# Optimization experiments

Hardware: AMD Instinct MI355X
Metric: run time of the kernel (lower is better)

The kernel has to match this reference:

```python
import jax, jax.numpy as jnp
import numpy as np

NEG_SLOPE = 0.01  # F.leaky_relu default
EPS = 1e-12       # F.normalize default eps

def _lrelu(h):
    return jnp.where(h > 0, h, NEG_SLOPE * h)

def setup_inputs() -> dict:
    key = jax.random.key(0)
    ks = jax.random.split(key, 16)
    N, E, D = 100000, 800000, 64
    x = jax.random.normal(ks[0], (N, D), dtype=jnp.float32)
    src = jax.random.randint(ks[1], (E,), 0, N, dtype=jnp.int32)
    dst = jax.random.randint(ks[2], (E,), 0, N, dtype=jnp.int32)
    def lin(k, fo, fi):
        k1, k2 = jax.random.split(k)
        s = 1.0 / np.sqrt(fi)
        w = jax.random.uniform(k1, (fo, fi), jnp.float32, -s, s)
        b = jax.random.uniform(k2, (fo,), jnp.float32, -s, s)
        return w, b
    w1, b1 = lin(ks[3], 256, D)
    w2, b2 = lin(ks[4], 128, 256)
    w3, b3 = lin(ks[5], 64, 128)
    w4, b4 = lin(ks[6], 1, 64)
    w_self, _ = lin(ks[7], D, D)   # SAGEConv fc_self (no bias)
    w_neigh, _ = lin(ks[8], D, D)  # SAGEConv fc_neigh (no bias)
    bias = jnp.zeros((D,), jnp.float32)  # SAGEConv bias param
    return dict(x=x, src=src, dst=dst, w1=w1, b1=b1, w2=w2, b2=b2,
                w3=w3, b3=b3, w4=w4, b4=b4,
                w_self=w_self, w_neigh=w_neigh, bias=bias)

def reference(x, src, dst, w1, b1, w2, b2, w3, b3, w4, b4, w_self, w_neigh, bias):
    N = x.shape[0]
    # per-edge score MLP on (h_u - h_v)
    d = x[src] - x[dst]                       # [E, D]
    h = _lrelu(d @ w1.T + b1)                 # [E, 256]
    h = _lrelu(h @ w2.T + b2)                 # [E, 128]
    h = _lrelu(h @ w3.T + b3)                 # [E, 64]
    e = jax.nn.sigmoid(h @ w4.T + b4)         # [E, 1]
    # SAGEConv 'mean' with edge weights: mean over incoming edges of e * x_src
    msg = e * x[src]                          # [E, D]
    s = jax.ops.segment_sum(msg, dst, num_segments=N)               # [N, D]
    deg = jax.ops.segment_sum(jnp.ones((src.shape[0],), x.dtype), dst,
                              num_segments=N)                        # [N]
    neigh = s / jnp.maximum(deg, 1.0)[:, None]
    A = x @ w_self.T + neigh @ w_neigh.T + bias
    A = _lrelu(A)
    norm = jnp.maximum(jnp.linalg.norm(A, axis=1, keepdims=True), EPS)
    A = A / norm
    return A, e
```

## Files before the change

kernel.cpp:

```cpp
#include <hip/hip_runtime.h>
#include <hip/hip_bf16.h>

typedef unsigned short u16;
typedef unsigned int   u32;
typedef __attribute__((ext_vector_type(8))) short short8;
typedef __attribute__((ext_vector_type(4))) float f32x4;

__device__ __forceinline__ u16 f2bf(float f) {
  u32 u = __float_as_uint(f);
  u += 0x7FFFu + ((u >> 16) & 1u);
  return (u16)(u >> 16);
}
__device__ __forceinline__ float bf2f(u16 h) { return __uint_as_float(((u32)h) << 16); }
__device__ __forceinline__ u32 pk2(float lo, float hi) {
  union { __hip_bfloat162 h; u32 u; } c;
  c.h = __float22bfloat162_rn(make_float2(lo, hi));
  return c.u;
}
__device__ __forceinline__ float lrelu(float v) { return v > 0.f ? v : 0.01f * v; }

__host__ __device__ __forceinline__ int sig(int c) {
  return ((c >> 5) << 5) | ((c & 12) << 1) | (((c >> 4) & 1) << 2) | (c & 3);
}

union U8 { u32 w[4]; short8 v; };

#define MFMA16(A, B, C) __builtin_amdgcn_mfma_f32_16x16x32_bf16(A, B, C, 0, 0, 0)

#define W2_BASE 2048
#define W3_BASE 6144
#define NCHUNK8 7168


__global__ __launch_bounds__(1024) void edge_mlp(
    const float* __restrict__ x, const int* __restrict__ src, const int* __restrict__ dst,
    const short8* __restrict__ wcat,
    const float* __restrict__ b1p, const float* __restrict__ b2p, const float* __restrict__ b3p,
    const float* __restrict__ w4p, const float* __restrict__ b4,
    const int* __restrict__ rowptr, int* __restrict__ cursor,
    u16* __restrict__ msgbuf, float* __restrict__ eout, int E)
{
  __shared__ short8 ldsw[NCHUNK8];
  const int tid  = threadIdx.x;
  const int lane = tid & 63;
  const int wv   = tid >> 6;
  const int g    = lane >> 4;
  const int r    = lane & 15;
  const int eb   = (blockIdx.x * 16 + wv) * 32;
  const int e0   = eb + r, e1 = eb + 16 + r;
  const int ec0  = e0 < E ? e0 : E - 1;
  const int ec1  = e1 < E ? e1 : E - 1;
  const int sn0 = src[ec0], dn0 = dst[ec0];
  const int sn1 = src[ec1], dn1 = dst[ec1];
  const float b4v = b4[0];

  const float* xsr0 = x + (size_t)sn0 * 64 + 8 * g;
  const float* xdr0 = x + (size_t)dn0 * 64 + 8 * g;
  const float* xsr1 = x + (size_t)sn1 * 64 + 8 * g;
  const float* xdr1 = x + (size_t)dn1 * 64 + 8 * g;
  const float4 a0s0 = *(const float4*)(xsr0),      a0s1 = *(const float4*)(xsr0 + 4);
  const float4 a0s2 = *(const float4*)(xsr0 + 32), a0s3 = *(const float4*)(xsr0 + 36);
  const float4 a0d0 = *(const float4*)(xdr0),      a0d1 = *(const float4*)(xdr0 + 4);
  const float4 a0d2 = *(const float4*)(xdr0 + 32), a0d3 = *(const float4*)(xdr0 + 36);
  const float4 a1s0 = *(const float4*)(xsr1),      a1s1 = *(const float4*)(xsr1 + 4);
  const float4 a1s2 = *(const float4*)(xsr1 + 32), a1s3 = *(const float4*)(xsr1 + 36);
  const float4 a1d0 = *(const float4*)(xdr1),      a1d1 = *(const float4*)(xdr1 + 4);
  const float4 a1d2 = *(const float4*)(xdr1 + 32), a1d3 = *(const float4*)(xdr1 + 36);

  {
    const short8* gp = wcat + wv * 64 + lane;
    short8*       lp = ldsw + wv * 64;
#pragma unroll
    for (int i = 0; i < 7; i++) {
      __builtin_amdgcn_global_load_lds(
          (const __attribute__((address_space(1))) u32*)(gp + i * 1024),
          (__attribute__((address_space(3))) u32*)(lp + i * 1024), 16, 0, 0);
    }
  }
  __syncthreads();

  U8 bA0, bB0, bA1, bB1;
  bA0.w[0] = pk2(a0s0.x - a0d0.x, a0s0.y - a0d0.y);
  bA0.w[1] = pk2(a0s0.z - a0d0.z, a0s0.w - a0d0.w);
  bA0.w[2] = pk2(a0s1.x - a0d1.x, a0s1.y - a0d1.y);
  bA0.w[3] = pk2(a0s1.z - a0d1.z, a0s1.w - a0d1.w);
  bB0.w[0] = pk2(a0s2.x - a0d2.x, a0s2.y - a0d2.y);
  bB0.w[1] = pk2(a0s2.z - a0d2.z, a0s2.w - a0d2.w);
  bB0.w[2] = pk2(a0s3.x - a0d3.x, a0s3.y - a0d3.y);
  bB0.w[3] = pk2(a0s3.z - a0d3.z, a0s3.w - a0d3.w);
  bA1.w[0] = pk2(a1s0.x - a1d0.x, a1s0.y - a1d0.y);
  bA1.w[1] = pk2(a1s0.z - a1d0.z, a1s0.w - a1d0.w);
  bA1.w[2] = pk2(a1s1.x - a1d1.x, a1s1.y - a1d1.y);
  bA1.w[3] = pk2(a1s1.z - a1d1.z, a1s1.w - a1d1.w);
  bB1.w[0] = pk2(a1s2.x - a1d2.x, a1s2.y - a1d2.y);
  bB1.w[1] = pk2(a1s2.z - a1d2.z, a1s2.w - a1d2.w);
  bB1.w[2] = pk2(a1s3.x - a1d3.x, a1s3.y - a1d3.y);
  bB1.w[3] = pk2(a1s3.z - a1d3.z, a1s3.w - a1d3.w);

  u32 h1a[32], h1b[32];
  {
    const float* b1l = b1p + 4 * g;
#pragma unroll
    for (int t = 0; t < 16; t++) {
      short8 a0 = ldsw[(t * 2 + 0) * 64 + lane];
      short8 a1 = ldsw[(t * 2 + 1) * 64 + lane];
      f32x4 p = {}, q = {};
      p = MFMA16(a0, bA0.v, p); p = MFMA16(a1, bB0.v, p);
      q = MFMA16(a0, bA1.v, q); q = MFMA16(a1, bB1.v, q);
      float4 bb = *(const float4*)(b1l + 16 * t);
      h1a[2 * t]     = pk2(lrelu(p[0] + bb.x), lrelu(p[1] + bb.y));
      h1a[2 * t + 1] = pk2(lrelu(p[2] + bb.z), lrelu(p[3] + bb.w));
      h1b[2 * t]     = pk2(lrelu(q[0] + bb.x), lrelu(q[1] + bb.y));
      h1b[2 * t + 1] = pk2(lrelu(q[2] + bb.z), lrelu(q[3] + bb.w));
    }
  }

  u32 h2a[16], h2b[16];
  {
    const float* b2l = b2p + 4 * g;
#pragma unroll
    for (int t = 0; t < 8; t++) {
      f32x4 p = {}, q = {};
#pragma unroll
      for (int s = 0; s < 8; s++) {
        short8 a = ldsw[W2_BASE + (t * 8 + s) * 64 + lane];
        U8 f0, f1;
        f0.w[0] = h1a[4 * s + 0]; f0.w[1] = h1a[4 * s + 1];
        f0.w[2] = h1a[4 * s + 2]; f0.w[3] = h1a[4 * s + 3];
        f1.w[0] = h1b[4 * s + 0]; f1.w[1] = h1b[4 * s + 1];
        f1.w[2] = h1b[4 * s + 2]; f1.w[3] = h1b[4 * s + 3];
        p = MFMA16(a, f0.v, p);
        q = MFMA16(a, f1.v, q);
      }
      float4 bb = *(const float4*)(b2l + 16 * t);
      h2a[2 * t]     = pk2(lrelu(p[0] + bb.x), lrelu(p[1] + bb.y));
      h2a[2 * t + 1] = pk2(lrelu(p[2] + bb.z), lrelu(p[3] + bb.w));
      h2b[2 * t]     = pk2(lrelu(q[0] + bb.x), lrelu(q[1] + bb.y));
      h2b[2 * t + 1] = pk2(lrelu(q[2] + bb.z), lrelu(q[3] + bb.w));
    }
  }

  float dot0 = 0.f, dot1 = 0.f;
  {
    const float* b3l = b3p + 4 * g;
    const float* w4l = w4p + 4 * g;
#pragma unroll
    for (int t = 0; t < 4; t++) {
      f32x4 p = {}, q = {};
#pragma unroll
      for (int s = 0; s < 4; s++) {
        short8 a = ldsw[W3_BASE + (t * 4 + s) * 64 + lane];
        U8 f0, f1;
        f0.w[0] = h2a[4 * s + 0]; f0.w[1] = h2a[4 * s + 1];
        f0.w[2] = h2a[4 * s + 2]; f0.w[3] = h2a[4 * s + 3];
        f1.w[0] = h2b[4 * s + 0]; f1.w[1] = h2b[4 * s + 1];
        f1.w[2] = h2b[4 * s + 2]; f1.w[3] = h2b[4 * s + 3];
        p = MFMA16(a, f0.v, p);
        q = MFMA16(a, f1.v, q);
      }
      float4 bb = *(const float4*)(b3l + 16 * t);
      float4 ww = *(const float4*)(w4l + 16 * t);
      dot0 += lrelu(p[0] + bb.x) * ww.x + lrelu(p[1] + bb.y) * ww.y
            + lrelu(p[2] + bb.z) * ww.z + lrelu(p[3] + bb.w) * ww.w;
      dot1 += lrelu(q[0] + bb.x) * ww.x + lrelu(q[1] + bb.y) * ww.y
            + lrelu(q[2] + bb.z) * ww.z + lrelu(q[3] + bb.w) * ww.w;
    }
  }
  dot0 += __shfl_xor(dot0, 16); dot0 += __shfl_xor(dot0, 32);
  dot1 += __shfl_xor(dot1, 16); dot1 += __shfl_xor(dot1, 32);
  const float ev0 = 1.f / (1.f + __expf(-(dot0 + b4v)));
  const float ev1 = 1.f / (1.f + __expf(-(dot1 + b4v)));

  int pos0 = 0, pos1 = 0;
  if (g == 0) {
    if (e0 < E) { eout[e0] = ev0; pos0 = rowptr[dn0] + atomicAdd(&cursor[dn0], 1); }
    if (e1 < E) { eout[e1] = ev1; pos1 = rowptr[dn1] + atomicAdd(&cursor[dn1], 1); }
  }
  pos0 = __shfl(pos0, r);
  pos1 = __shfl(pos1, r);
  if (e0 < E) {
    u16* mp = msgbuf + (size_t)pos0 * 64 + g * 16;
    U8 m;
    m.w[0] = pk2(ev0 * a0s0.x, ev0 * a0s0.y);
    m.w[1] = pk2(ev0 * a0s0.z, ev0 * a0s0.w);
    m.w[2] = pk2(ev0 * a0s1.x, ev0 * a0s1.y);
    m.w[3] = pk2(ev0 * a0s1.z, ev0 * a0s1.w);
    *(short8*)(mp) = m.v;
    m.w[0] = pk2(ev0 * a0s2.x, ev0 * a0s2.y);
    m.w[1] = pk2(ev0 * a0s2.z, ev0 * a0s2.w);
    m.w[2] = pk2(ev0 * a0s3.x, ev0 * a0s3.y);
    m.w[3] = pk2(ev0 * a0s3.z, ev0 * a0s3.w);
    *(short8*)(mp + 8) = m.v;
  }
  if (e1 < E) {
    u16* mp = msgbuf + (size_t)pos1 * 64 + g * 16;
    U8 m;
    m.w[0] = pk2(ev1 * a1s0.x, ev1 * a1s0.y);
    m.w[1] = pk2(ev1 * a1s0.z, ev1 * a1s0.w);
    m.w[2] = pk2(ev1 * a1s1.x, ev1 * a1s1.y);
    m.w[3] = pk2(ev1 * a1s1.z, ev1 * a1s1.w);
    *(short8*)(mp) = m.v;
    m.w[0] = pk2(ev1 * a1s2.x, ev1 * a1s2.y);
    m.w[1] = pk2(ev1 * a1s2.z, ev1 * a1s2.w);
    m.w[2] = pk2(ev1 * a1s3.x, ev1 * a1s3.y);
    m.w[3] = pk2(ev1 * a1s3.z, ev1 * a1s3.w);
    *(short8*)(mp + 8) = m.v;
  }
}

__global__ void deg_hist(const int* __restrict__ dst, int* __restrict__ degi, int E)
{
  const int i = blockIdx.x * 256 + threadIdx.x;
  if (i < E) atomicAdd(&degi[dst[i]], 1);
}

__global__ void scan_part(const int* __restrict__ degi, int* __restrict__ rowptr,
                          int* __restrict__ bsum, int N)
{
  __shared__ int wsum[4];
  const int tid = threadIdx.x, lane = tid & 63, w = tid >> 6;
  const int base = blockIdx.x * 1024 + tid * 4;
  int d0 = 0, d1 = 0, d2 = 0, d3 = 0;
  if (base + 3 < N) {
    int4 v = *(const int4*)(degi + base);
    d0 = v.x; d1 = v.y; d2 = v.z; d3 = v.w;
  } else {
    if (base < N)     d0 = degi[base];
    if (base + 1 < N) d1 = degi[base + 1];
    if (base + 2 < N) d2 = degi[base + 2];
    if (base + 3 < N) d3 = degi[base + 3];
  }
  const int ts = d0 + d1 + d2 + d3;
  int sc = ts;
#pragma unroll
  for (int o = 1; o < 64; o <<= 1) { int v = __shfl_up(sc, o); if (lane >= o) sc += v; }
  if (lane == 63) wsum[w] = sc;
  __syncthreads();
  int woff = 0;
  for (int i = 0; i < w; i++) woff += wsum[i];
  const int ex = woff + sc - ts;
  if (base < N)     rowptr[base]     = ex;
  if (base + 1 < N) rowptr[base + 1] = ex + d0;
  if (base + 2 < N) rowptr[base + 2] = ex + d0 + d1;
  if (base + 3 < N) rowptr[base + 3] = ex + d0 + d1 + d2;
  if (tid == 255) bsum[blockIdx.x] = woff + sc;
}

__global__ void scan_bsum(int* __restrict__ bsum, int nb)
{
  __shared__ int wsum[4];
  const int tid = threadIdx.x, lane = tid & 63, w = tid >> 6;
  const int v = tid < nb ? bsum[tid] : 0;
  int sc = v;
#pragma unroll
  for (int o = 1; o < 64; o <<= 1) { int t = __shfl_up(sc, o); if (lane >= o) sc += t; }
  if (lane == 63) wsum[w] = sc;
  __syncthreads();
  int woff = 0;
  for (int i = 0; i < w; i++) woff += wsum[i];
  if (tid < nb) bsum[tid] = woff + sc - v;
}

__global__ void scan_add(int* __restrict__ rowptr, const int* __restrict__ bsum,
                         int* __restrict__ cursor, int N, int E)
{
  const int base = blockIdx.x * 1024 + threadIdx.x * 4;
  const int off = bsum[blockIdx.x];
#pragma unroll
  for (int i = 0; i < 4; i++)
    if (base + i < N) { rowptr[base + i] += off; cursor[base + i] = 0; }
  if (blockIdx.x == 0 && threadIdx.x == 0) rowptr[N] = E;
}

__global__ __launch_bounds__(256, 4) void node_agg_mfma(
    const float* __restrict__ x, const u16* __restrict__ msgbuf,
    const int* __restrict__ rowptr, const short8* __restrict__ wfin,
    const float* __restrict__ bias, float* __restrict__ A, int N)
{
  __shared__ short8 ldsW[1024];
  __shared__ float  nbuf[4][16][68];
  const int tid = threadIdx.x, wv = tid >> 6, lane = tid & 63;
  const int g = lane >> 4, r = lane & 15;
  for (int i = tid; i < 1024; i += 256) ldsW[i] = wfin[i];

  const int n0 = (blockIdx.x * 4 + wv) * 16;
  const int nr = (n0 + r) < N ? (n0 + r) : N - 1;
  const float* xp = x + (size_t)nr * 64 + 8 * g;
  const float4 xf0 = *(const float4*)(xp);
  const float4 xf1 = *(const float4*)(xp + 4);
  const float4 xf2 = *(const float4*)(xp + 32);
  const float4 xf3 = *(const float4*)(xp + 36);
  int rp = 0;
  if (lane < 17) rp = rowptr[min(n0 + lane, N)];
  const int cch = (((lane >> 3) & 1) << 5) | ((lane >> 4) << 3) | (lane & 7);
  for (int rr = 0; rr < 16; rr++) {
    const int s = __shfl(rp, rr);
    const int t = __shfl(rp, rr + 1);
    float acc = 0.f;
    for (int j = s; j < t; j += 4) {
      const int j1 = (j + 1 < t) ? j + 1 : j;
      const int j2 = (j + 2 < t) ? j + 2 : j;
      const int j3 = (j + 3 < t) ? j + 3 : j;
      const float v0 = bf2f(msgbuf[(size_t)j  * 64 + lane]);
      const float v1 = bf2f(msgbuf[(size_t)j1 * 64 + lane]);
      const float v2 = bf2f(msgbuf[(size_t)j2 * 64 + lane]);
      const float v3 = bf2f(msgbuf[(size_t)j3 * 64 + lane]);
      const float m1 = (j + 1 < t) ? 1.f : 0.f;
      const float m2 = (j + 2 < t) ? 1.f : 0.f;
      const float m3 = (j + 3 < t) ? 1.f : 0.f;
      acc += v0 + m1 * v1 + m2 * v2 + m3 * v3;
    }
    const float inv = 1.f / fmaxf((float)(t - s), 1.f);
    nbuf[wv][rr][cch] = acc * inv;
  }
  __syncthreads();

  U8 bf0, bf1, bf2q, bf3q;
  bf0.w[0] = pk2(xf0.x, xf0.y); bf0.w[1] = pk2(xf0.z, xf0.w);
  bf0.w[2] = pk2(xf1.x, xf1.y); bf0.w[3] = pk2(xf1.z, xf1.w);
  bf1.w[0] = pk2(xf2.x, xf2.y); bf1.w[1] = pk2(xf2.z, xf2.w);
  bf1.w[2] = pk2(xf3.x, xf3.y); bf1.w[3] = pk2(xf3.z, xf3.w);
  {
    const float* nb = nbuf[wv][r];
    const float4 n0v = *(const float4*)(nb + 8 * g);
    const float4 n1v = *(const float4*)(nb + 8 * g + 4);
    const float4 n2v = *(const float4*)(nb + 32 + 8 * g);
    const float4 n3v = *(const float4*)(nb + 32 + 8 * g + 4);
    bf2q.w[0] = pk2(n0v.x, n0v.y); bf2q.w[1] = pk2(n0v.z, n0v.w);
    bf2q.w[2] = pk2(n1v.x, n1v.y); bf2q.w[3] = pk2(n1v.z, n1v.w);
    bf3q.w[0] = pk2(n2v.x, n2v.y); bf3q.w[1] = pk2(n2v.z, n2v.w);
    bf3q.w[2] = pk2(n3v.x, n3v.y); bf3q.w[3] = pk2(n3v.z, n3v.w);
  }

  f32x4 acct[4] = {};
#pragma unroll
  for (int t = 0; t < 4; t++) {
    acct[t] = MFMA16(ldsW[(t * 4 + 0) * 64 + lane], bf0.v,  acct[t]);
    acct[t] = MFMA16(ldsW[(t * 4 + 1) * 64 + lane], bf1.v,  acct[t]);
    acct[t] = MFMA16(ldsW[(t * 4 + 2) * 64 + lane], bf2q.v, acct[t]);
    acct[t] = MFMA16(ldsW[(t * 4 + 3) * 64 + lane], bf3q.v, acct[t]);
  }

  f32x4 av[4];
  float ss = 0.f;
#pragma unroll
  for (int t = 0; t < 4; t++) {
    const float4 bb = *(const float4*)(bias + 16 * t + 4 * g);
    av[t][0] = lrelu(acct[t][0] + bb.x);
    av[t][1] = lrelu(acct[t][1] + bb.y);
    av[t][2] = lrelu(acct[t][2] + bb.z);
    av[t][3] = lrelu(acct[t][3] + bb.w);
    ss += av[t][0] * av[t][0] + av[t][1] * av[t][1]
        + av[t][2] * av[t][2] + av[t][3] * av[t][3];
  }
  ss += __shfl_xor(ss, 16); ss += __shfl_xor(ss, 32);
  const float rn = 1.f / fmaxf(sqrtf(ss), 1e-12f);
  if (n0 + r < N) {
    float* ap = A + (size_t)(n0 + r) * 64 + 4 * g;
#pragma unroll
    for (int t = 0; t < 4; t++) {
      float4 o;
      o.x = av[t][0] * rn; o.y = av[t][1] * rn;
      o.z = av[t][2] * rn; o.w = av[t][3] * rn;
      *(float4*)(ap + 16 * t) = o;
    }
  }
}

__global__ void convert_w(const float* __restrict__ w1, const float* __restrict__ w2,
                          const float* __restrict__ w3,
                          const float* __restrict__ b1, const float* __restrict__ b2,
                          const float* __restrict__ b3, const float* __restrict__ w4,
                          const float* __restrict__ w_self, const float* __restrict__ w_neigh,
                          u16* __restrict__ wcat, u16* __restrict__ wfin,
                          float* __restrict__ b1p, float* __restrict__ b2p,
                          float* __restrict__ b3p, float* __restrict__ w4p)
{
  const int idx = blockIdx.x * 256 + threadIdx.x;
  if (idx < 57344) {
    const float* w; int K, nsteps, loc;
    if (idx < 16384)      { loc = idx;         w = w1; K = 64;  nsteps = 2; }
    else if (idx < 49152) { loc = idx - 16384; w = w2; K = 256; nsteps = 8; }
    else                  { loc = idx - 49152; w = w3; K = 128; nsteps = 4; }
    const int chunk = loc >> 9;
    const int lane  = (loc >> 3) & 63;
    const int j     = loc & 7;
    const int t = chunk / nsteps, s = chunk % nsteps;
    const int m = sig(t * 16 + (lane & 15));
    const int k = s * 32 + (lane >> 4) * 8 + j;
    wcat[idx] = f2bf(w[m * K + k]);
  } else if (idx < 65536) {
    const int o = idx - 57344;
    const int c = o >> 9, lane = (o >> 3) & 63, j = o & 7;
    const int t = c >> 2, s = c & 3;
    const int m = 16 * t + (lane & 15);
    const int k = 32 * s + ((lane >> 4) << 3) + j;
    wfin[o] = f2bf(k < 64 ? w_self[m * 64 + k] : w_neigh[m * 64 + (k - 64)]);
  }
  if (idx < 256) b1p[idx] = b1[sig(idx)];
  if (idx < 128) b2p[idx] = b2[sig(idx)];
  if (idx < 64)  { b3p[idx] = b3[sig(idx)]; w4p[idx] = w4[sig(idx)]; }
}

extern "C" void kernel_launch(void* const* d_in, const int* in_sizes, int n_in,
                              void* d_out, int out_size, void* d_ws, size_t ws_size,
                              hipStream_t stream)
{
  const float* x       = (const float*)d_in[0];
  const int*   src     = (const int*)d_in[1];
  const int*   dst     = (const int*)d_in[2];
  const float* w1      = (const float*)d_in[3];
  const float* b1      = (const float*)d_in[4];
  const float* w2      = (const float*)d_in[5];
  const float* b2      = (const float*)d_in[6];
  const float* w3      = (const float*)d_in[7];
  const float* b3      = (const float*)d_in[8];
  const float* w4      = (const float*)d_in[9];
  const float* b4      = (const float*)d_in[10];
  const float* w_self  = (const float*)d_in[11];
  const float* w_neigh = (const float*)d_in[12];
  const float* bias    = (const float*)d_in[13];

  const int N = in_sizes[0] / 64;
  const int E = in_sizes[1];

  float* A    = (float*)d_out;
  float* eout = (float*)d_out + (size_t)N * 64;

  char* ws = (char*)d_ws;
  size_t off = 0;
  auto alloc = [&](size_t bytes) {
    void* p = ws + off;
    off = (off + bytes + 255) & ~(size_t)255;
    return p;
  };
  int*    degi   = (int*)alloc((size_t)N * 4);
  int*    rowptr = (int*)alloc((size_t)(N + 1) * 4);
  int*    cursor = (int*)alloc((size_t)N * 4);
  int*    bsum   = (int*)alloc(1024 * 4);
  short8* wcat   = (short8*)alloc((size_t)57344 * 2);
  short8* wfin   = (short8*)alloc((size_t)8192 * 2);
  float*  b1p    = (float*)alloc(256 * 4);
  float*  b2p    = (float*)alloc(128 * 4);
  float*  b3p    = (float*)alloc(64 * 4);
  float*  w4p    = (float*)alloc(64 * 4);
  u16*    msgbuf = (u16*)alloc((size_t)E * 128);

  hipMemsetAsync(degi, 0, (size_t)N * sizeof(int), stream);

  convert_w<<<256, 256, 0, stream>>>(w1, w2, w3, b1, b2, b3, w4, w_self, w_neigh,
                                     (u16*)wcat, (u16*)wfin, b1p, b2p, b3p, w4p);

  deg_hist<<<(E + 255) / 256, 256, 0, stream>>>(dst, degi, E);

  const int nsb = (N + 1023) / 1024;
  scan_part<<<nsb, 256, 0, stream>>>(degi, rowptr, bsum, N);
  scan_bsum<<<1, 256, 0, stream>>>(bsum, nsb);
  scan_add<<<nsb, 256, 0, stream>>>(rowptr, bsum, cursor, N, E);

  const int nblk = (E + 511) / 512;
  edge_mlp<<<nblk, 1024, 0, stream>>>(x, src, dst, wcat, b1p, b2p, b3p, w4p, b4,
                                      rowptr, cursor, msgbuf, eout, E);

  const int nblk2 = (N + 63) / 64;
  node_agg_mfma<<<nblk2, 256, 0, stream>>>(x, msgbuf, rowptr, wfin, bias, A, N);
}
```

Measured before the change: 337.9 us.

## Stream layer-1 weights from global, shrink LDS and block size for occupancy

Layer-1 weights are now read directly from global memory (L2/L1 cached) with a one-step register prefetch, instead of being staged in LDS. The LDS staging of the layer-2 and layer-3 weights overlaps with layer-1 compute, and the barrier moves after layer 1. Blocks shrink from 1024 to 512 threads with launch_bounds(512,2), which cuts LDS per block so more blocks can be resident. Source features are packed to bf16 early so fewer fp32 registers stay live across the MLP. The trade-off is more global weight traffic per wave, slightly different message rounding (double bf16 rounding), and possible register spilling under the tighter bound.

```diff
diff --git a/kernel.cpp b/kernel.cpp
--- a/kernel.cpp
+++ b/kernel.cpp
@@ -17,6 +17,8 @@
   c.h = __float22bfloat162_rn(make_float2(lo, hi));
   return c.u;
 }
+__device__ __forceinline__ float lo16f(u32 u) { return __uint_as_float(u << 16); }
+__device__ __forceinline__ float hi16f(u32 u) { return __uint_as_float(u & 0xffff0000u); }
 __device__ __forceinline__ float lrelu(float v) { return v > 0.f ? v : 0.01f * v; }
 
 __host__ __device__ __forceinline__ int sig(int c) {
@@ -27,12 +29,11 @@
 
 #define MFMA16(A, B, C) __builtin_amdgcn_mfma_f32_16x16x32_bf16(A, B, C, 0, 0, 0)
 
-#define W2_BASE 2048
-#define W3_BASE 6144
-#define NCHUNK8 7168
-
-
-__global__ __launch_bounds__(1024) void edge_mlp(
+#define LDS_CHUNK8 5120
+#define LDS_W3     4096
+
+
+__global__ __launch_bounds__(512, 2) void edge_mlp(
     const float* __restrict__ x, const int* __restrict__ src, const int* __restrict__ dst,
     const short8* __restrict__ wcat,
     const float* __restrict__ b1p, const float* __restrict__ b2p, const float* __restrict__ b3p,
@@ -40,13 +41,13 @@
     const int* __restrict__ rowptr, int* __restrict__ cursor,
     u16* __restrict__ msgbuf, float* __restrict__ eout, int E)
 {
-  __shared__ short8 ldsw[NCHUNK8];
+  __shared__ short8 ldsw[LDS_CHUNK8];
   const int tid  = threadIdx.x;
   const int lane = tid & 63;
   const int wv   = tid >> 6;
   const int g    = lane >> 4;
   const int r    = lane & 15;
-  const int eb   = (blockIdx.x * 16 + wv) * 32;
+  const int eb   = (blockIdx.x * 8 + wv) * 32;
   const int e0   = eb + r, e1 = eb + 16 + r;
   const int ec0  = e0 < E ? e0 : E - 1;
   const int ec1  = e1 < E ? e1 : E - 1;
@@ -67,19 +68,21 @@
   const float4 a1d0 = *(const float4*)(xdr1),      a1d1 = *(const float4*)(xdr1 + 4);
   const float4 a1d2 = *(const float4*)(xdr1 + 32), a1d3 = *(const float4*)(xdr1 + 36);
 
+  short8 na0 = wcat[lane];
+  short8 na1 = wcat[64 + lane];
+
   {
-    const short8* gp = wcat + wv * 64 + lane;
+    const short8* gp = wcat + 2048 + wv * 64 + lane;
     short8*       lp = ldsw + wv * 64;
 #pragma unroll
-    for (int i = 0; i < 7; i++) {
+    for (int i = 0; i < 10; i++) {
       __builtin_amdgcn_global_load_lds(
-          (const __attribute__((address_space(1))) u32*)(gp + i * 1024),
-          (__attribute__((address_space(3))) u32*)(lp + i * 1024), 16, 0, 0);
-    }
-  }
-  __syncthreads();
-
-  U8 bA0, bB0, bA1, bB1;
+          (const __attribute__((address_space(1))) u32*)(gp + i * 512),
+          (__attribute__((address_space(3))) u32*)(lp + i * 512), 16, 0, 0);
+    }
+  }
+
+  U8 bA0, bB0, bA1, bB1, sA0lo, sA0hi, sA1lo, sA1hi;
   bA0.w[0] = pk2(a0s0.x - a0d0.x, a0s0.y - a0d0.y);
   bA0.w[1] = pk2(a0s0.z - a0d0.z, a0s0.w - a0d0.w);
   bA0.w[2] = pk2(a0s1.x - a0d1.x, a0s1.y - a0d1.y);
@@ -96,14 +99,25 @@
   bB1.w[1] = pk2(a1s2.z - a1d2.z, a1s2.w - a1d2.w);
   bB1.w[2] = pk2(a1s3.x - a1d3.x, a1s3.y - a1d3.y);
   bB1.w[3] = pk2(a1s3.z - a1d3.z, a1s3.w - a1d3.w);
+  sA0lo.w[0] = pk2(a0s0.x, a0s0.y); sA0lo.w[1] = pk2(a0s0.z, a0s0.w);
+  sA0lo.w[2] = pk2(a0s1.x, a0s1.y); sA0lo.w[3] = pk2(a0s1.z, a0s1.w);
+  sA0hi.w[0] = pk2(a0s2.x, a0s2.y); sA0hi.w[1] = pk2(a0s2.z, a0s2.w);
+  sA0hi.w[2] = pk2(a0s3.x, a0s3.y); sA0hi.w[3] = pk2(a0s3.z, a0s3.w);
+  sA1lo.w[0] = pk2(a1s0.x, a1s0.y); sA1lo.w[1] = pk2(a1s0.z, a1s0.w);
+  sA1lo.w[2] = pk2(a1s1.x, a1s1.y); sA1lo.w[3] = pk2(a1s1.z, a1s1.w);
+  sA1hi.w[0] = pk2(a1s2.x, a1s2.y); sA1hi.w[1] = pk2(a1s2.z, a1s2.w);
+  sA1hi.w[2] = pk2(a1s3.x, a1s3.y); sA1hi.w[3] = pk2(a1s3.z, a1s3.w);
 
   u32 h1a[32], h1b[32];
   {
     const float* b1l = b1p + 4 * g;
 #pragma unroll
     for (int t = 0; t < 16; t++) {
-      short8 a0 = ldsw[(t * 2 + 0) * 64 + lane];
-      short8 a1 = ldsw[(t * 2 + 1) * 64 + lane];
+      short8 a0 = na0, a1 = na1;
+      if (t < 15) {
+        na0 = wcat[(2 * t + 2) * 64 + lane];
+        na1 = wcat[(2 * t + 3) * 64 + lane];
+      }
       f32x4 p = {}, q = {};
       p = MFMA16(a0, bA0.v, p); p = MFMA16(a1, bB0.v, p);
       q = MFMA16(a0, bA1.v, q); q = MFMA16(a1, bB1.v, q);
@@ -114,6 +128,7 @@
       h1b[2 * t + 1] = pk2(lrelu(q[2] + bb.z), lrelu(q[3] + bb.w));
     }
   }
+  __syncthreads();
 
   u32 h2a[16], h2b[16];
   {
@@ -123,7 +138,7 @@
       f32x4 p = {}, q = {};
 #pragma unroll
       for (int s = 0; s < 8; s++) {
-        short8 a = ldsw[W2_BASE + (t * 8 + s) * 64 + lane];
+        short8 a = ldsw[(t * 8 + s) * 64 + lane];
         U8 f0, f1;
         f0.w[0] = h1a[4 * s + 0]; f0.w[1] = h1a[4 * s + 1];
         f0.w[2] = h1a[4 * s + 2]; f0.w[3] = h1a[4 * s + 3];
@@ -149,7 +164,7 @@
       f32x4 p = {}, q = {};
 #pragma unroll
       for (int s = 0; s < 4; s++) {
-        short8 a = ldsw[W3_BASE + (t * 4 + s) * 64 + lane];
+        short8 a = ldsw[LDS_W3 + (t * 4 + s) * 64 + lane];
         U8 f0, f1;
         f0.w[0] = h2a[4 * s + 0]; f0.w[1] = h2a[4 * s + 1];
         f0.w[2] = h2a[4 * s + 2]; f0.w[3] = h2a[4 * s + 3];
@@ -181,29 +196,29 @@
   if (e0 < E) {
     u16* mp = msgbuf + (size_t)pos0 * 64 + g * 16;
     U8 m;
-    m.w[0] = pk2(ev0 * a0s0.x, ev0 * a0s0.y);
-    m.w[1] = pk2(ev0 * a0s0.z, ev0 * a0s0.w);
-    m.w[2] = pk2(ev0 * a0s1.x, ev0 * a0s1.y);
-    m.w[3] = pk2(ev0 * a0s1.z, ev0 * a0s1.w);
+    m.w[0] = pk2(ev0 * lo16f(sA0lo.w[0]), ev0 * hi16f(sA0lo.w[0]));
+    m.w[1] = pk2(ev0 * lo16f(sA0lo.w[1]), ev0 * hi16f(sA0lo.w[1]));
+    m.w[2] = pk2(ev0 * lo16f(sA0lo.w[2]), ev0 * hi16f(sA0lo.w[2]));
+    m.w[3] = pk2(ev0 * lo16f(sA0lo.w[3]), ev0 * hi16f(sA0lo.w[3]));
     *(short8*)(mp) = m.v;
-    m.w[0] = pk2(ev0 * a0s2.x, ev0 * a0s2.y);
-    m.w[1] = pk2(ev0 * a0s2.z, ev0 * a0s2.w);
-    m.w[2] = pk2(ev0 * a0s3.x, ev0 * a0s3.y);
-    m.w[3] = pk2(ev0 * a0s3.z, ev0 * a0s3.w);
+    m.w[0] = pk2(ev0 * lo16f(sA0hi.w[0]), ev0 * hi16f(sA0hi.w[0]));
+    m.w[1] = pk2(ev0 * lo16f(sA0hi.w[1]), ev0 * hi16f(sA0hi.w[1]));
+    m.w[2] = pk2(ev0 * lo16f(sA0hi.w[2]), ev0 * hi16f(sA0hi.w[2]));
+    m.w[3] = pk2(ev0 * lo16f(sA0hi.w[3]), ev0 * hi16f(sA0hi.w[3]));
     *(short8*)(mp + 8) = m.v;
   }
   if (e1 < E) {
     u16* mp = msgbuf + (size_t)pos1 * 64 + g * 16;
     U8 m;
-    m.w[0] = pk2(ev1 * a1s0.x, ev1 * a1s0.y);
-    m.w[1] = pk2(ev1 * a1s0.z, ev1 * a1s0.w);
-    m.w[2] = pk2(ev1 * a1s1.x, ev1 * a1s1.y);
-    m.w[3] = pk2(ev1 * a1s1.z, ev1 * a1s1.w);
+    m.w[0] = pk2(ev1 * lo16f(sA1lo.w[0]), ev1 * hi16f(sA1lo.w[0]));
+    m.w[1] = pk2(ev1 * lo16f(sA1lo.w[1]), ev1 * hi16f(sA1lo.w[1]));
+    m.w[2] = pk2(ev1 * lo16f(sA1lo.w[2]), ev1 * hi16f(sA1lo.w[2]));
+    m.w[3] = pk2(ev1 * lo16f(sA1lo.w[3]), ev1 * hi16f(sA1lo.w[3]));
     *(short8*)(mp) = m.v;
-    m.w[0] = pk2(ev1 * a1s2.x, ev1 * a1s2.y);
-    m.w[1] = pk2(ev1 * a1s2.z, ev1 * a1s2.w);
-    m.w[2] = pk2(ev1 * a1s3.x, ev1 * a1s3.y);
-    m.w[3] = pk2(ev1 * a1s3.z, ev1 * a1s3.w);
+    m.w[0] = pk2(ev1 * lo16f(sA1hi.w[0]), ev1 * hi16f(sA1hi.w[0]));
+    m.w[1] = pk2(ev1 * lo16f(sA1hi.w[1]), ev1 * hi16f(sA1hi.w[1]));
+    m.w[2] = pk2(ev1 * lo16f(sA1hi.w[2]), ev1 * hi16f(sA1hi.w[2]));
+    m.w[3] = pk2(ev1 * lo16f(sA1hi.w[3]), ev1 * hi16f(sA1hi.w[3]));
     *(short8*)(mp + 8) = m.v;
   }
 }
@@ -458,9 +473,9 @@
   scan_bsum<<<1, 256, 0, stream>>>(bsum, nsb);
   scan_add<<<nsb, 256, 0, stream>>>(rowptr, bsum, cursor, N, E);
 
-  const int nblk = (E + 511) / 512;
-  edge_mlp<<<nblk, 1024, 0, stream>>>(x, src, dst, wcat, b1p, b2p, b3p, w4p, b4,
-                                      rowptr, cursor, msgbuf, eout, E);
+  const int nblk = (E + 255) / 256;
+  edge_mlp<<<nblk, 512, 0, stream>>>(x, src, dst, wcat, b1p, b2p, b3p, w4p, b4,
+                                     rowptr, cursor, msgbuf, eout, E);
 
   const int nblk2 = (N + 63) / 64;
   node_agg_mfma<<<nblk2, 256, 0, stream>>>(x, msgbuf, rowptr, wfin, bias, A, N);
```

New measurement: 334.5 us. No clear change (-1.0%).
